# Kernel tuning notes

Measured on AMD Instinct MI355X. Metric: run time of the kernel, lower is better.

## Reference

```python
import jax, jax.numpy as jnp
import numpy as np

D = 2560
H = 64
HD = D // H  # 40
TE = 512
FF = 4 * D  # 10240
EPS = 1e-5


def _ln(x, eps=EPS):
    # fp32 layernorm, no affine
    x32 = x.astype(jnp.float32)
    mu = jnp.mean(x32, axis=-1, keepdims=True)
    var = jnp.var(x32, axis=-1, keepdims=True)
    return ((x32 - mu) * jax.lax.rsqrt(var + eps)).astype(x.dtype)


def _rope(x, cos, sin):
    # x: [B, H, S_img, HD]; cos/sin: [S_img, HD]
    half = x.shape[-1] // 2
    xr, xi = x[..., :half], x[..., half:]
    x_rot = jnp.concatenate([-xi, xr], axis=-1)
    c = cos[None, None]
    s = sin[None, None]
    return (x.astype(jnp.float32) * c + x_rot.astype(jnp.float32) * s).astype(x.dtype)


def setup_inputs() -> dict:
    key = jax.random.key(0)
    ks = jax.random.split(key, 20)
    f = jnp.float32
    inp = {
        "hidden_states": jax.random.normal(ks[0], (1, 1024, D), f),
        "encoder_hidden_states": jax.random.normal(ks[1], (1, 128, D), f),
        "time_embed": jax.random.normal(ks[2], (1, TE), f),
        "rope_cos": jax.random.uniform(ks[3], (1024, HD), f),
        "rope_sin": jax.random.uniform(ks[4], (1024, HD), f),
        # AdaLayerNormZero linear: time_embed_dim -> 12*D
        "ada_w": jax.random.normal(ks[5], (TE, 12 * D), f) * 0.02,
        "ada_b": jnp.zeros((12 * D,), f),
        # attention projections (stored [in, out])
        "wq": jax.random.normal(ks[6], (D, D), f) * 0.02,
        "bq": jnp.zeros((D,), f),
        "wk": jax.random.normal(ks[7], (D, D), f) * 0.02,
        "bk": jnp.zeros((D,), f),
        "wv": jax.random.normal(ks[8], (D, D), f) * 0.02,
        "bv": jnp.zeros((D,), f),
        "wo": jax.random.normal(ks[9], (D, D), f) * 0.02,
        "bo": jnp.zeros((D,), f),
        # feedforward (shared for img and context streams)
        "w1": jax.random.normal(ks[10], (D, FF), f) * 0.02,
        "b1": jnp.zeros((FF,), f),
        "w2": jax.random.normal(ks[11], (FF, D), f) * 0.02,
        "b2": jnp.zeros((D,), f),
    }
    return inp


def _block(hidden_states, encoder_hidden_states, time_embed, rope_cos, rope_sin,
           ada_w, ada_b, wq, bq, wk, bk, wv, bv, wo, bo, w1, b1, w2, b2):
    B, T, _ = encoder_hidden_states.shape

    # --- AdaLayerNormZero ---
    emb = time_embed @ ada_w + ada_b  # [B, 12*D]
    (shift_msa, c_shift_msa, scale_msa, c_scale_msa, gate_msa, c_gate_msa,
     shift_mlp, c_shift_mlp, scale_mlp, c_scale_mlp, gate_mlp, c_gate_mlp) = jnp.split(emb, 12, axis=1)
    u = lambda v: v[:, None, :]  # [B,1,D]

    norm_h = _ln(hidden_states) * (1 + u(scale_msa)) + u(shift_msa)
    norm_e = _ln(encoder_hidden_states) * (1 + u(c_scale_msa)) + u(c_shift_msa)

    # --- SelfAttention on concatenated [text, image] sequence ---
    x = jnp.concatenate([norm_e, norm_h], axis=1)  # [B,S,D]
    S = x.shape[1]
    def heads(y):
        return y.reshape(B, S, H, HD).transpose(0, 2, 1, 3)  # [B,H,S,HD]
    q = heads(x @ wq + bq)
    k = heads(x @ wk + bk)
    v = heads(x @ wv + bv)
    q = _ln(q)  # fp32 QK-norm over head_dim
    k = _ln(k)
    # partial RoPE on image tokens only
    q = q.at[:, :, T:, :].set(_rope(q[:, :, T:, :], rope_cos, rope_sin))
    k = k.at[:, :, T:, :].set(_rope(k[:, :, T:, :], rope_cos, rope_sin))

    scores = jnp.einsum('bhqd,bhkd->bhqk', q, k) / np.sqrt(HD).astype(np.float32)
    attn = jax.nn.softmax(scores, axis=-1)
    o = jnp.einsum('bhqk,bhkd->bhqd', attn, v)  # [B,H,S,HD]
    o = o.transpose(0, 2, 1, 3).reshape(B, S, D)
    o = o @ wo + bo
    attn_e, attn_h = o[:, :T], o[:, T:]

    # --- residual with attn gates ---
    hidden_states = hidden_states + attn_h * u(gate_msa)
    encoder_hidden_states = encoder_hidden_states + attn_e * u(c_gate_msa)

    # --- MLP with AdaLN modulation + gates ---
    nh = _ln(hidden_states) * (1 + u(scale_mlp)) + u(shift_mlp)
    ne = _ln(encoder_hidden_states) * (1 + u(c_scale_mlp)) + u(c_shift_mlp)
    ff = lambda y: jax.nn.gelu(y @ w1 + b1, approximate=True) @ w2 + b2
    hidden_states = hidden_states + ff(nh) * u(gate_mlp)
    encoder_hidden_states = encoder_hidden_states + ff(ne) * u(c_gate_mlp)
    return hidden_states, encoder_hidden_states


def reference(hidden_states, encoder_hidden_states, time_embed, rope_cos, rope_sin,
              ada_w, ada_b, wq, bq, wk, bk, wv, bv, wo, bo, w1, b1, w2, b2):
    return _block(hidden_states, encoder_hidden_states, time_embed, rope_cos, rope_sin,
                  ada_w, ada_b, wq, bq, wk, bk, wv, bv, wo, bo, w1, b1, w2, b2)
```

## Files before the change

kernel.cpp:

```cpp
#include <hip/hip_runtime.h>
#include <stdint.h>

#define D 2560
#define NH 64
#define HD 40
#define TE_ 512
#define FFD 10240
#define TENC 128
#define THID 1024
#define SEQ 1152

typedef __bf16 bf16_t;
typedef __bf16 bf16x8 __attribute__((ext_vector_type(8)));
typedef float  f32x4  __attribute__((ext_vector_type(4)));

__device__ __forceinline__ void gld_lds16(const void* g, void* l) {
  __builtin_amdgcn_global_load_lds((__attribute__((address_space(1))) void*)(g),
                                   (__attribute__((address_space(3))) void*)(l), 16, 0, 0);
}

__device__ __forceinline__ void wtrans_tile(const float* __restrict__ W, bf16_t* __restrict__ Wt,
                                            int K, int N, int bk, int bn, int tid,
                                            float* tile ) {
  #pragma unroll
  for (int i = 0; i < 4; ++i) {
    int c = i * 256 + tid;
    int r = c >> 4, q = c & 15;
    f32x4 v = *(const f32x4*)(W + (size_t)(bk * 64 + r) * N + bn * 64 + q * 4);
    tile[r * 65 + q * 4 + 0] = v[0]; tile[r * 65 + q * 4 + 1] = v[1];
    tile[r * 65 + q * 4 + 2] = v[2]; tile[r * 65 + q * 4 + 3] = v[3];
  }
  __syncthreads();
  #pragma unroll
  for (int i = 0; i < 2; ++i) {
    int c = i * 256 + tid;
    int n = c >> 3, kc = c & 7;
    bf16x8 o;
    #pragma unroll
    for (int j = 0; j < 8; ++j) o[j] = (bf16_t)tile[(kc * 8 + j) * 65 + n];
    *(bf16x8*)(Wt + (size_t)(bn * 64 + n) * K + bk * 64 + kc * 8) = o;
  }
}

__global__ __launch_bounds__(256) void prep1(
    const float* __restrict__ te, const float* __restrict__ aw, const float* __restrict__ ab,
    float* __restrict__ emb,
    const float* __restrict__ wq, const float* __restrict__ wk,
    const float* __restrict__ wv, const float* __restrict__ wo,
    bf16_t* __restrict__ wqkvT, bf16_t* __restrict__ woT,
    const float* __restrict__ bq, const float* __restrict__ bk, const float* __restrict__ bv,
    float* __restrict__ bqkv, bf16_t* __restrict__ vt) {
  __shared__ float tile[64 * 65];
  const int b = blockIdx.x, t = threadIdx.x;
  if (b < 120) {
    int j = b * 256 + t;
    float acc = ab[j];
    #pragma unroll 8
    for (int k = 0; k < TE_; ++k) acc = fmaf(te[k], aw[(size_t)k * (12 * D) + j], acc);
    emb[j] = acc;
  } else if (b < 1720) {
    int l = b - 120;  wtrans_tile(wq, wqkvT,                     D, D, l % 40, l / 40, t, tile);
  } else if (b < 3320) {
    int l = b - 1720; wtrans_tile(wk, wqkvT + (size_t)D * D,     D, D, l % 40, l / 40, t, tile);
  } else if (b < 4920) {
    int l = b - 3320; wtrans_tile(wv, wqkvT + (size_t)2 * D * D, D, D, l % 40, l / 40, t, tile);
  } else if (b < 6520) {
    int l = b - 4920; wtrans_tile(wo, woT,                       D, D, l % 40, l / 40, t, tile);
  } else if (b < 6550) {
    int i = (b - 6520) * 256 + t;
    bqkv[i] = i < D ? bq[i] : (i < 2 * D ? bk[i - D] : bv[i - 2 * D]);
  } else {
    int i = (b - 6550) * 256 + t;
    bf16x8 z = {};
    *(bf16x8*)(vt + (size_t)i * 8) = z;
  }
}

__global__ void ln_mod(const float* __restrict__ hid, const float* __restrict__ enc,
                       const float* __restrict__ emb, bf16_t* __restrict__ out,
                       int shift_h, int scale_h, int shift_e, int scale_e) {
  int row = blockIdx.x, tid = threadIdx.x;
  const float *src, *sc, *sh;
  if (row < TENC) { src = enc + (size_t)row * D;          sc = emb + scale_e * D; sh = emb + shift_e * D; }
  else            { src = hid + (size_t)(row - TENC) * D; sc = emb + scale_h * D; sh = emb + shift_h * D; }
  float v[10], s = 0.f, s2 = 0.f;
  #pragma unroll
  for (int i = 0; i < 10; ++i) { v[i] = src[tid + i * 256]; s += v[i]; s2 += v[i] * v[i]; }
  #pragma unroll
  for (int o = 32; o > 0; o >>= 1) { s += __shfl_down(s, o); s2 += __shfl_down(s2, o); }
  __shared__ float red[8];
  int wv = tid >> 6, ln = tid & 63;
  if (ln == 0) { red[wv] = s; red[4 + wv] = s2; }
  __syncthreads();
  s  = red[0] + red[1] + red[2] + red[3];
  s2 = red[4] + red[5] + red[6] + red[7];
  float mean = s * (1.f / D);
  float rstd = rsqrtf(s2 * (1.f / D) - mean * mean + 1e-5f);
  #pragma unroll
  for (int i = 0; i < 10; ++i) {
    int c = tid + i * 256;
    out[(size_t)row * D + c] = (bf16_t)((v[i] - mean) * rstd * (1.f + sc[c]) + sh[c]);
  }
}

template<int EPI>
__device__ __forceinline__ void gemm_body(
    bf16_t* As, bf16_t* Bs,
    const bf16_t* __restrict__ A, const bf16_t* __restrict__ Bt,
    const float* __restrict__ bias, int Kld, int ksteps, int N, int nM, int nMN,
    int nwg, int orig,
    float* __restrict__ outq, float* __restrict__ outk, bf16_t* __restrict__ outv,
    bf16_t* __restrict__ outb, float* __restrict__ outp) {
  const int q8 = nwg >> 3, r8 = nwg & 7;
  const int xcd = orig & 7, pos = orig >> 3;
  const int wg = (xcd < r8 ? xcd * (q8 + 1) : r8 * (q8 + 1) + (xcd - r8) * q8) + pos;
  const int part = wg / nMN, rest = wg - part * nMN;
  const int bm = rest % nM, bn = rest / nM;
  const int m0 = bm * 128, n0 = bn * 128;
  const int kbase = part * ksteps;
  const int tid = threadIdx.x, wv = tid >> 6, ln = tid & 63;
  const int wr = wv >> 1, wc = wv & 1, lr = ln & 15, lg = ln >> 4;

  f32x4 acc[4][4];
  const f32x4 zero = {0.f, 0.f, 0.f, 0.f};
  #pragma unroll
  for (int m = 0; m < 4; ++m)
    #pragma unroll
    for (int n = 0; n < 4; ++n) acc[m][n] = zero;

  for (int t = 0; t < ksteps; ++t) {
    const int k0 = (kbase + t) << 6;
    __syncthreads();
    #pragma unroll
    for (int i = 0; i < 4; ++i) {
      int g = wv * 4 + i;
      int s = g * 64 + ln;
      int r = s >> 3, ks = s & 7;
      gld_lds16(A + (size_t)(m0 + r) * Kld + k0 + ((ks ^ (r & 7)) << 3), &As[g * 512]);
    }
    #pragma unroll
    for (int i = 0; i < 4; ++i) {
      int g = wv * 4 + i;
      int s = g * 64 + ln;
      int r = s >> 3, ks = s & 7;
      gld_lds16(Bt + (size_t)(n0 + r) * Kld + k0 + ((ks ^ (r & 7)) << 3), &Bs[g * 512]);
    }
    __syncthreads();
    #pragma unroll
    for (int ks2 = 0; ks2 < 2; ++ks2) {
      int ko = ks2 * 4 + lg;
      bf16x8 af[4], bfr[4];
      #pragma unroll
      for (int m = 0; m < 4; ++m) {
        int r = wr * 64 + m * 16 + lr;
        af[m] = *(const bf16x8*)&As[r * 64 + ((ko ^ (r & 7)) << 3)];
      }
      #pragma unroll
      for (int n = 0; n < 4; ++n) {
        int c = wc * 64 + n * 16 + lr;
        bfr[n] = *(const bf16x8*)&Bs[c * 64 + ((ko ^ (c & 7)) << 3)];
      }
      #pragma unroll
      for (int m = 0; m < 4; ++m)
        #pragma unroll
        for (int n = 0; n < 4; ++n)
          acc[m][n] = __builtin_amdgcn_mfma_f32_16x16x32_bf16(af[m], bfr[n], acc[m][n], 0, 0, 0);
    }
  }

  #pragma unroll
  for (int m = 0; m < 4; ++m) {
    int row = m0 + wr * 64 + m * 16 + (lg << 2);
    #pragma unroll
    for (int n = 0; n < 4; ++n) {
      int col = n0 + wc * 64 + n * 16 + lr;
      float bv = (EPI == 4) ? 0.f : bias[col];
      #pragma unroll
      for (int r = 0; r < 4; ++r) {
        float val = acc[m][n][r] + bv;
        int rr = row + r;
        if (EPI == 0) {
          int which = col / D, cc = col - which * D;
          int h = cc / HD, dd = cc - h * HD;
          if (which == 0)      outq[(size_t)h * SEQ * HD + (size_t)rr * HD + dd] = val;
          else if (which == 1) outk[(size_t)h * SEQ * HD + (size_t)rr * HD + dd] = val;
          else                 outv[((size_t)h * 48 + dd) * SEQ + rr] = (bf16_t)val;
        } else if (EPI == 1) {
          float z = 0.7978845608028654f * (val + 0.044715f * val * val * val);
          float t2 = 1.f - 2.f / (__expf(2.f * z) + 1.f);
          outb[(size_t)rr * N + col] = (bf16_t)(0.5f * val * (1.f + t2));
        } else {
          outp[(size_t)part * SEQ * N + (size_t)rr * N + col] = val;
        }
      }
    }
  }
}

template<int EPI>
__global__ __launch_bounds__(256, 4) void gemm4(
    const bf16_t* __restrict__ A, const bf16_t* __restrict__ Bt,
    const float* __restrict__ bias, int Kld, int ksteps, int N, int nM, int nMN,
    float* __restrict__ outq, float* __restrict__ outk, bf16_t* __restrict__ outv,
    bf16_t* __restrict__ outb, float* __restrict__ outp) {
  __shared__ bf16_t As[128 * 64];
  __shared__ bf16_t Bs[128 * 64];
  gemm_body<EPI>(As, Bs, A, Bt, bias, Kld, ksteps, N, nM, nMN, gridDim.x, blockIdx.x,
                 outq, outk, outv, outb, outp);
}

__global__ __launch_bounds__(256, 4) void qkv_plus(
    const bf16_t* __restrict__ A, const bf16_t* __restrict__ wqkvT,
    const float* __restrict__ bqkv,
    float* __restrict__ outq, float* __restrict__ outk, bf16_t* __restrict__ outv,
    const float* __restrict__ w1, bf16_t* __restrict__ w1T,
    const float* __restrict__ w2, bf16_t* __restrict__ w2T) {
  __shared__ char smem[32768] __attribute__((aligned(16)));
  const int b = blockIdx.x;
  if (b < 540) {
    gemm_body<0>((bf16_t*)smem, (bf16_t*)(smem + 16384), A, wqkvT, bqkv,
                 D, 40, 3 * D, 9, 540, 540, b, outq, outk, outv, nullptr, nullptr);
  } else if (b < 6940) {
    int l = b - 540;
    wtrans_tile(w1, w1T, D, FFD, l % 40, l / 40, threadIdx.x, (float*)smem);
  } else {
    int l = b - 6940;
    wtrans_tile(w2, w2T, FFD, D, l % 160, l / 160, threadIdx.x, (float*)smem);
  }
}

template<int P>
__global__ void redk(const float* __restrict__ parts, const float* __restrict__ bias,
                     const float* __restrict__ emb, int gate_h, int gate_e,
                     const float* __restrict__ res_h, const float* __restrict__ res_e,
                     float* __restrict__ out_h, float* __restrict__ out_e) {
  int idx = blockIdx.x * 256 + threadIdx.x;
  int row = idx / (D / 4), col = (idx - row * (D / 4)) * 4;
  f32x4 s = *(const f32x4*)(bias + col);
  #pragma unroll
  for (int p = 0; p < P; ++p)
    s += *(const f32x4*)(parts + (size_t)p * SEQ * D + (size_t)row * D + col);
  const float* res; float* out; int g;
  int r2;
  if (row < TENC) { res = res_e; out = out_e; g = gate_e; r2 = row; }
  else            { res = res_h; out = out_h; g = gate_h; r2 = row - TENC; }
  f32x4 g4 = *(const f32x4*)(emb + (size_t)g * D + col);
  f32x4 rr4 = *(const f32x4*)(res + (size_t)r2 * D + col);
  f32x4 o;
  #pragma unroll
  for (int j = 0; j < 4; ++j) o[j] = rr4[j] + s[j] * g4[j];
  *(f32x4*)(out + (size_t)r2 * D + col) = o;
}

template<int P>
__global__ __launch_bounds__(256) void redk_ln(
    const float* __restrict__ parts, const float* __restrict__ bias,
    const float* __restrict__ emb, int gate_h, int gate_e,
    int shift_h, int scale_h, int shift_e, int scale_e,
    const float* __restrict__ res_h, const float* __restrict__ res_e,
    float* __restrict__ out_h, float* __restrict__ out_e, bf16_t* __restrict__ xout) {
  int row = blockIdx.x, tid = threadIdx.x;
  const float* res; float* out; int g, sh, sc; int r2;
  if (row < TENC) { res = res_e; out = out_e; g = gate_e; sh = shift_e; sc = scale_e; r2 = row; }
  else            { res = res_h; out = out_h; g = gate_h; sh = shift_h; sc = scale_h; r2 = row - TENC; }
  float v[10], s = 0.f, s2 = 0.f;
  #pragma unroll
  for (int i = 0; i < 10; ++i) {
    int c = tid + i * 256;
    float val = bias[c];
    #pragma unroll
    for (int p = 0; p < P; ++p) val += parts[(size_t)p * SEQ * D + (size_t)row * D + c];
    val = res[(size_t)r2 * D + c] + val * emb[(size_t)g * D + c];
    out[(size_t)r2 * D + c] = val;
    v[i] = val; s += val; s2 += val * val;
  }
  #pragma unroll
  for (int o = 32; o > 0; o >>= 1) { s += __shfl_down(s, o); s2 += __shfl_down(s2, o); }
  __shared__ float red[8];
  int wvv = tid >> 6, lnn = tid & 63;
  if (lnn == 0) { red[wvv] = s; red[4 + wvv] = s2; }
  __syncthreads();
  s  = red[0] + red[1] + red[2] + red[3];
  s2 = red[4] + red[5] + red[6] + red[7];
  float mean = s * (1.f / D);
  float rstd = rsqrtf(s2 * (1.f / D) - mean * mean + 1e-5f);
  #pragma unroll
  for (int i = 0; i < 10; ++i) {
    int c = tid + i * 256;
    xout[(size_t)row * D + c] =
        (bf16_t)((v[i] - mean) * rstd * (1.f + emb[(size_t)sc * D + c]) + emb[(size_t)sh * D + c]);
  }
}

__global__ void qk_post(const float* __restrict__ qh, const float* __restrict__ kh,
                        const float* __restrict__ rc, const float* __restrict__ rs,
                        bf16_t* __restrict__ qb, bf16_t* __restrict__ kb) {
  int r = blockIdx.x * 128 + threadIdx.x;
  int h = blockIdx.y;
  float cs[HD], sn[HD];
  bool rope = (r >= TENC);
  if (rope) {
    const float* cp = rc + (size_t)(r - TENC) * HD;
    const float* sp = rs + (size_t)(r - TENC) * HD;
    #pragma unroll
    for (int d = 0; d < HD; ++d) { cs[d] = cp[d]; sn[d] = sp[d]; }
  }
  #pragma unroll
  for (int which = 0; which < 2; ++which) {
    const float* base = (which == 0 ? qh : kh) + (size_t)h * SEQ * HD + (size_t)r * HD;
    bf16_t* dst = (which == 0 ? qb : kb) + ((size_t)h * SEQ + r) * 64;
    float v[HD], s = 0.f, s2 = 0.f;
    #pragma unroll
    for (int d = 0; d < HD; ++d) { v[d] = base[d]; s += v[d]; }
    float mean = s * (1.f / HD);
    #pragma unroll
    for (int d = 0; d < HD; ++d) { float x = v[d] - mean; v[d] = x; s2 += x * x; }
    float rstd = rsqrtf(s2 * (1.f / HD) + 1e-5f);
    #pragma unroll
    for (int d = 0; d < HD; ++d) v[d] *= rstd;
    if (rope) {
      #pragma unroll
      for (int d = 0; d < HD / 2; ++d) {
        float lo = v[d], hi = v[d + 20];
        v[d]      = lo * cs[d]      - hi * sn[d];
        v[d + 20] = hi * cs[d + 20] + lo * sn[d + 20];
      }
    }
    float qs = (which == 0) ? 0.15811388300841897f : 1.f;
    #pragma unroll
    for (int d = 0; d < HD; ++d) dst[d] = (bf16_t)(v[d] * qs);
    #pragma unroll
    for (int d = HD; d < 64; ++d) dst[d] = (bf16_t)0.f;
  }
}

__global__ __launch_bounds__(256) void attn_mfma(
    const bf16_t* __restrict__ qb, const bf16_t* __restrict__ kb,
    const bf16_t* __restrict__ vt, bf16_t* __restrict__ obf) {
  __shared__ bf16_t Ks[64 * 64];
  __shared__ bf16_t Vs[48 * 64];
  __shared__ bf16_t Ps[4][16 * 64];
  const int h = blockIdx.y;
  const int tid = threadIdx.x, wv = tid >> 6, ln = tid & 63;
  const int qbase = blockIdx.x * 64 + wv * 16;
  const int lr = ln & 15, lg = ln >> 4;

  bf16x8 af[2];
  {
    const bf16_t* qp = qb + ((size_t)h * SEQ + qbase + lr) * 64 + lg * 8;
    af[0] = *(const bf16x8*)(qp);
    af[1] = *(const bf16x8*)(qp + 32);
  }
  const f32x4 zero = {0.f, 0.f, 0.f, 0.f};
  f32x4 acc[3];
  acc[0] = zero; acc[1] = zero; acc[2] = zero;
  float mrow[4], lrow[4];
  #pragma unroll
  for (int r = 0; r < 4; ++r) { mrow[r] = -1e30f; lrow[r] = 0.f; }

  const bf16_t* kbh = kb + (size_t)h * SEQ * 64;
  const bf16_t* vth = vt + (size_t)h * 48 * SEQ;

  for (int kv0 = 0; kv0 < SEQ; kv0 += 64) {
    __syncthreads();
    #pragma unroll
    for (int i = 0; i < 2; ++i) {
      int g = wv * 2 + i;
      int slot = g * 64 + ln;
      int kr = slot >> 3, so = slot & 7;
      gld_lds16(kbh + (size_t)(kv0 + kr) * 64 + ((so ^ (kr & 7)) << 3), &Ks[g * 512]);
    }
    #pragma unroll
    for (int i = 0; i < 2; ++i) {
      int g = wv + 4 * i;
      if (g < 6) {
        int slot = g * 64 + ln;
        int dr = slot >> 3, so = slot & 7;
        gld_lds16(vth + (size_t)dr * SEQ + kv0 + ((so ^ (dr & 7)) << 3), &Vs[g * 512]);
      }
    }
    __syncthreads();
    f32x4 s[4];
    #pragma unroll
    for (int nt = 0; nt < 4; ++nt) {
      s[nt] = zero;
      int kvr = nt * 16 + lr;
      #pragma unroll
      for (int kk = 0; kk < 2; ++kk) {
        bf16x8 bk = *(const bf16x8*)&Ks[kvr * 64 + (((kk * 4 + lg) ^ (kvr & 7)) << 3)];
        s[nt] = __builtin_amdgcn_mfma_f32_16x16x32_bf16(af[kk], bk, s[nt], 0, 0, 0);
      }
    }
    float pn[4][4];
    #pragma unroll
    for (int r = 0; r < 4; ++r) {
      float tm = fmaxf(fmaxf(s[0][r], s[1][r]), fmaxf(s[2][r], s[3][r]));
      #pragma unroll
      for (int o = 8; o > 0; o >>= 1) tm = fmaxf(tm, __shfl_xor(tm, o));
      float mn = fmaxf(mrow[r], tm);
      float scl = __expf(mrow[r] - mn);
      mrow[r] = mn;
      float ts = 0.f;
      #pragma unroll
      for (int nt = 0; nt < 4; ++nt) { pn[nt][r] = __expf(s[nt][r] - mn); ts += pn[nt][r]; }
      #pragma unroll
      for (int o = 8; o > 0; o >>= 1) ts += __shfl_xor(ts, o);
      lrow[r] = lrow[r] * scl + ts;
      acc[0][r] *= scl; acc[1][r] *= scl; acc[2][r] *= scl;
    }
    #pragma unroll
    for (int nt = 0; nt < 4; ++nt)
      #pragma unroll
      for (int r = 0; r < 4; ++r) {
        int q = lg * 4 + r;
        int kv = nt * 16 + lr;
        Ps[wv][q * 64 + ((((kv >> 3) ^ (q & 7)) << 3) | (kv & 7))] = (bf16_t)pn[nt][r];
      }
    bf16x8 pa[2];
    #pragma unroll
    for (int kk = 0; kk < 2; ++kk)
      pa[kk] = *(const bf16x8*)&Ps[wv][lr * 64 + (((kk * 4 + lg) ^ (lr & 7)) << 3)];
    #pragma unroll
    for (int dt = 0; dt < 3; ++dt) {
      #pragma unroll
      for (int kk = 0; kk < 2; ++kk) {
        int dr = dt * 16 + lr;
        bf16x8 bv = *(const bf16x8*)&Vs[dr * 64 + (((kk * 4 + lg) ^ (dr & 7)) << 3)];
        acc[dt] = __builtin_amdgcn_mfma_f32_16x16x32_bf16(pa[kk], bv, acc[dt], 0, 0, 0);
      }
    }
  }
  #pragma unroll
  for (int dt = 0; dt < 3; ++dt) {
    int d = dt * 16 + lr;
    if (d < HD) {
      #pragma unroll
      for (int r = 0; r < 4; ++r) {
        int q = qbase + lg * 4 + r;
        obf[(size_t)q * D + h * HD + d] = (bf16_t)(acc[dt][r] / lrow[r]);
      }
    }
  }
}

extern "C" void kernel_launch(void* const* d_in, const int* in_sizes, int n_in,
                              void* d_out, int out_size, void* d_ws, size_t ws_size,
                              hipStream_t stream) {
  const float* hid = (const float*)d_in[0];
  const float* enc = (const float*)d_in[1];
  const float* tem = (const float*)d_in[2];
  const float* rc  = (const float*)d_in[3];
  const float* rs  = (const float*)d_in[4];
  const float* aw  = (const float*)d_in[5];
  const float* ab  = (const float*)d_in[6];
  const float* wq  = (const float*)d_in[7];
  const float* bq  = (const float*)d_in[8];
  const float* wk  = (const float*)d_in[9];
  const float* bk  = (const float*)d_in[10];
  const float* wvv = (const float*)d_in[11];
  const float* bv  = (const float*)d_in[12];
  const float* wo  = (const float*)d_in[13];
  const float* bo  = (const float*)d_in[14];
  const float* w1  = (const float*)d_in[15];
  const float* b1  = (const float*)d_in[16];
  const float* w2  = (const float*)d_in[17];
  const float* b2  = (const float*)d_in[18];
  float* out_hid = (float*)d_out;
  float* out_enc = out_hid + (size_t)THID * D;

  char* ws = (char*)d_ws;
  size_t off = 0;
  auto alloc = [&](size_t b) { char* p = ws + off; off += (b + 255) & ~(size_t)255; return p; };
  float*  emb  = (float*) alloc((size_t)12 * D * 4);
  bf16_t* xln  = (bf16_t*)alloc((size_t)SEQ * D * 2);
  float*  qh   = (float*) alloc((size_t)NH * SEQ * HD * 4);
  float*  kh   = (float*) alloc((size_t)NH * SEQ * HD * 4);
  bf16_t* vt   = (bf16_t*)alloc((size_t)NH * 48 * SEQ * 2);
  bf16_t* qbb  = (bf16_t*)alloc((size_t)NH * SEQ * 64 * 2);
  bf16_t* kbb  = (bf16_t*)alloc((size_t)NH * SEQ * 64 * 2);
  bf16_t* wqkvT= (bf16_t*)alloc((size_t)3 * D * D * 2);
  bf16_t* woT  = (bf16_t*)alloc((size_t)D * D * 2);
  bf16_t* w1T  = (bf16_t*)alloc((size_t)FFD * D * 2);
  bf16_t* w2T  = (bf16_t*)alloc((size_t)D * FFD * 2);
  float*  bqkv = (float*) alloc((size_t)3 * D * 4);
  bf16_t* obf = xln;
  bf16_t* aff = (bf16_t*)qh;
  float*  h1  = (float*)qbb;
  float*  e1  = h1 + (size_t)THID * D;
  float*  oparts = (float*)wqkvT;
  float*  fparts = (float*)wqkvT;

  prep1<<<dim3(8278), dim3(256), 0, stream>>>(tem, aw, ab, emb, wq, wk, wvv, wo,
      wqkvT, woT, bq, bk, bv, bqkv, vt);
  ln_mod<<<dim3(SEQ), dim3(256), 0, stream>>>(hid, enc, emb, xln, 0, 2, 1, 3);
  qkv_plus<<<dim3(13340), dim3(256), 0, stream>>>(xln, wqkvT, bqkv, qh, kh, vt,
      w1, w1T, w2, w2T);
  qk_post<<<dim3(9, 64), dim3(128), 0, stream>>>(qh, kh, rc, rs, qbb, kbb);
  attn_mfma<<<dim3(18, 64), dim3(256), 0, stream>>>(qbb, kbb, vt, obf);
  gemm4<4><<<dim3(360), dim3(256), 0, stream>>>(obf, woT, nullptr, D, 20, D, 9, 180,
      nullptr, nullptr, nullptr, nullptr, oparts);
  redk_ln<2><<<dim3(SEQ), dim3(256), 0, stream>>>(oparts, bo, emb, 4, 5, 6, 8, 7, 9,
      hid, enc, h1, e1, xln);
  gemm4<1><<<dim3(720), dim3(256), 0, stream>>>(xln, w1T, b1, D, 40, FFD, 9, 720,
      nullptr, nullptr, nullptr, aff, nullptr);
  gemm4<4><<<dim3(720), dim3(256), 0, stream>>>(aff, w2T, nullptr, FFD, 40, D, 9, 180,
      nullptr, nullptr, nullptr, nullptr, fparts);
  redk<4><<<dim3(2880), dim3(256), 0, stream>>>(fparts, b2, emb, 10, 11, h1, e1, out_hid, out_enc);
}
```

Baseline: 475.1 us.

## Split-K QKV GEMM, fuse QK-norm/RoPE reduction, and rebalance weight transposes across kernels

The QKV GEMM now uses a two-way split-K, which doubles its workgroup count, and writes fp32 partial sums. A new row-wise kernel sums the partials, adds the bias, and applies per-head layernorm, RoPE, Q scaling and bf16 packing, replacing the old scattered epilogue and the separate qk_post kernel. The Wo transpose moves into the QKV launch, and the W1/W2 transposes are folded into the attention launch so they overlap with attention work. The split-K adds extra fp32 partial traffic, and qparts reuses the w1T buffer, so correctness depends on w1T being written only after qkv_red has consumed it.

```diff
diff --git a/kernel.cpp b/kernel.cpp
--- a/kernel.cpp
+++ b/kernel.cpp
@@ -45,9 +45,8 @@
 __global__ __launch_bounds__(256) void prep1(
     const float* __restrict__ te, const float* __restrict__ aw, const float* __restrict__ ab,
     float* __restrict__ emb,
-    const float* __restrict__ wq, const float* __restrict__ wk,
-    const float* __restrict__ wv, const float* __restrict__ wo,
-    bf16_t* __restrict__ wqkvT, bf16_t* __restrict__ woT,
+    const float* __restrict__ wq, const float* __restrict__ wk, const float* __restrict__ wv,
+    bf16_t* __restrict__ wqkvT,
     const float* __restrict__ bq, const float* __restrict__ bk, const float* __restrict__ bv,
     float* __restrict__ bqkv, bf16_t* __restrict__ vt) {
   __shared__ float tile[64 * 65];
@@ -64,15 +63,14 @@
     int l = b - 1720; wtrans_tile(wk, wqkvT + (size_t)D * D,     D, D, l % 40, l / 40, t, tile);
   } else if (b < 4920) {
     int l = b - 3320; wtrans_tile(wv, wqkvT + (size_t)2 * D * D, D, D, l % 40, l / 40, t, tile);
-  } else if (b < 6520) {
-    int l = b - 4920; wtrans_tile(wo, woT,                       D, D, l % 40, l / 40, t, tile);
-  } else if (b < 6550) {
-    int i = (b - 6520) * 256 + t;
+  } else if (b < 4950) {
+    int i = (b - 4920) * 256 + t;
     bqkv[i] = i < D ? bq[i] : (i < 2 * D ? bk[i - D] : bv[i - 2 * D]);
   } else {
-    int i = (b - 6550) * 256 + t;
+    int i = (b - 4950) * 256 + t;
+    int h = i / 1152, g = i - h * 1152;
     bf16x8 z = {};
-    *(bf16x8*)(vt + (size_t)i * 8) = z;
+    *(bf16x8*)(vt + ((size_t)h * 48 + 40) * SEQ + g * 8) = z;
   }
 }
 
@@ -109,7 +107,6 @@
     const bf16_t* __restrict__ A, const bf16_t* __restrict__ Bt,
     const float* __restrict__ bias, int Kld, int ksteps, int N, int nM, int nMN,
     int nwg, int orig,
-    float* __restrict__ outq, float* __restrict__ outk, bf16_t* __restrict__ outv,
     bf16_t* __restrict__ outb, float* __restrict__ outp) {
   const int q8 = nwg >> 3, r8 = nwg & 7;
   const int xcd = orig & 7, pos = orig >> 3;
@@ -179,13 +176,7 @@
       for (int r = 0; r < 4; ++r) {
         float val = acc[m][n][r] + bv;
         int rr = row + r;
-        if (EPI == 0) {
-          int which = col / D, cc = col - which * D;
-          int h = cc / HD, dd = cc - h * HD;
-          if (which == 0)      outq[(size_t)h * SEQ * HD + (size_t)rr * HD + dd] = val;
-          else if (which == 1) outk[(size_t)h * SEQ * HD + (size_t)rr * HD + dd] = val;
-          else                 outv[((size_t)h * 48 + dd) * SEQ + rr] = (bf16_t)val;
-        } else if (EPI == 1) {
+        if (EPI == 1) {
           float z = 0.7978845608028654f * (val + 0.044715f * val * val * val);
           float t2 = 1.f - 2.f / (__expf(2.f * z) + 1.f);
           outb[(size_t)rr * N + col] = (bf16_t)(0.5f * val * (1.f + t2));
@@ -201,31 +192,93 @@
 __global__ __launch_bounds__(256, 4) void gemm4(
     const bf16_t* __restrict__ A, const bf16_t* __restrict__ Bt,
     const float* __restrict__ bias, int Kld, int ksteps, int N, int nM, int nMN,
-    float* __restrict__ outq, float* __restrict__ outk, bf16_t* __restrict__ outv,
     bf16_t* __restrict__ outb, float* __restrict__ outp) {
   __shared__ bf16_t As[128 * 64];
   __shared__ bf16_t Bs[128 * 64];
   gemm_body<EPI>(As, Bs, A, Bt, bias, Kld, ksteps, N, nM, nMN, gridDim.x, blockIdx.x,
-                 outq, outk, outv, outb, outp);
-}
-
-__global__ __launch_bounds__(256, 4) void qkv_plus(
+                 outb, outp);
+}
+
+__global__ __launch_bounds__(256, 4) void qkv_g(
     const bf16_t* __restrict__ A, const bf16_t* __restrict__ wqkvT,
-    const float* __restrict__ bqkv,
-    float* __restrict__ outq, float* __restrict__ outk, bf16_t* __restrict__ outv,
-    const float* __restrict__ w1, bf16_t* __restrict__ w1T,
-    const float* __restrict__ w2, bf16_t* __restrict__ w2T) {
+    float* __restrict__ qparts,
+    const float* __restrict__ wo, bf16_t* __restrict__ woT) {
   __shared__ char smem[32768] __attribute__((aligned(16)));
   const int b = blockIdx.x;
-  if (b < 540) {
-    gemm_body<0>((bf16_t*)smem, (bf16_t*)(smem + 16384), A, wqkvT, bqkv,
-                 D, 40, 3 * D, 9, 540, 540, b, outq, outk, outv, nullptr, nullptr);
-  } else if (b < 6940) {
-    int l = b - 540;
-    wtrans_tile(w1, w1T, D, FFD, l % 40, l / 40, threadIdx.x, (float*)smem);
+  if (b < 1080) {
+    gemm_body<4>((bf16_t*)smem, (bf16_t*)(smem + 16384), A, wqkvT, nullptr,
+                 D, 20, 3 * D, 9, 540, 1080, b, nullptr, qparts);
   } else {
-    int l = b - 6940;
-    wtrans_tile(w2, w2T, FFD, D, l % 160, l / 160, threadIdx.x, (float*)smem);
+    int l = b - 1080;
+    wtrans_tile(wo, woT, D, D, l % 40, l / 40, threadIdx.x, (float*)smem);
+  }
+}
+
+__global__ __launch_bounds__(256) void qkv_red(
+    const float* __restrict__ parts, const float* __restrict__ bqkv,
+    const float* __restrict__ rc, const float* __restrict__ rs,
+    bf16_t* __restrict__ qb, bf16_t* __restrict__ kb, bf16_t* __restrict__ vt) {
+  const int r = blockIdx.x, t = threadIdx.x;
+  const int h = t >> 2, sub = t & 3;
+  __shared__ float cs_s[HD], sn_s[HD];
+  const bool rope = (r >= TENC);
+  if (rope && t < 2 * HD) {
+    if (t < HD) cs_s[t] = rc[(size_t)(r - TENC) * HD + t];
+    else        sn_s[t - HD] = rs[(size_t)(r - TENC) * HD + (t - HD)];
+  }
+  const float* p0 = parts + (size_t)r * (3 * D);
+  const float* p1 = p0 + (size_t)SEQ * (3 * D);
+  const int cq = h * HD + sub * 10;
+  float q[10], k[10], v[10];
+  #pragma unroll
+  for (int j = 0; j < 10; ++j) {
+    q[j] = p0[cq + j] + p1[cq + j] + bqkv[cq + j];
+    k[j] = p0[D + cq + j] + p1[D + cq + j] + bqkv[D + cq + j];
+    v[j] = p0[2 * D + cq + j] + p1[2 * D + cq + j] + bqkv[2 * D + cq + j];
+  }
+  __syncthreads();
+  float qs = 0.f, qs2 = 0.f, ks = 0.f, ks2 = 0.f;
+  #pragma unroll
+  for (int j = 0; j < 10; ++j) { qs += q[j]; qs2 += q[j] * q[j]; ks += k[j]; ks2 += k[j] * k[j]; }
+  qs += __shfl_xor(qs, 1); qs += __shfl_xor(qs, 2);
+  qs2 += __shfl_xor(qs2, 1); qs2 += __shfl_xor(qs2, 2);
+  ks += __shfl_xor(ks, 1); ks += __shfl_xor(ks, 2);
+  ks2 += __shfl_xor(ks2, 1); ks2 += __shfl_xor(ks2, 2);
+  float qm = qs * (1.f / HD), km = ks * (1.f / HD);
+  float qr = rsqrtf(qs2 * (1.f / HD) - qm * qm + 1e-5f);
+  float kr = rsqrtf(ks2 * (1.f / HD) - km * km + 1e-5f);
+  #pragma unroll
+  for (int j = 0; j < 10; ++j) { q[j] = (q[j] - qm) * qr; k[j] = (k[j] - km) * kr; }
+  if (rope) {
+    float pq[10], pk[10];
+    #pragma unroll
+    for (int j = 0; j < 10; ++j) { pq[j] = __shfl_xor(q[j], 2); pk[j] = __shfl_xor(k[j], 2); }
+    #pragma unroll
+    for (int j = 0; j < 10; ++j) {
+      int d = sub * 10 + j;
+      float c = cs_s[d], s = sn_s[d];
+      if (d < 20) { q[j] = q[j] * c - pq[j] * s; k[j] = k[j] * c - pk[j] * s; }
+      else        { q[j] = q[j] * c + pq[j] * s; k[j] = k[j] * c + pk[j] * s; }
+    }
+  }
+  bf16_t* qd = qb + ((size_t)h * SEQ + r) * 64;
+  bf16_t* kd = kb + ((size_t)h * SEQ + r) * 64;
+  const float qscale = 0.15811388300841897f;
+  #pragma unroll
+  for (int j = 0; j < 10; ++j) {
+    int d = sub * 10 + j;
+    qd[d] = (bf16_t)(q[j] * qscale);
+    kd[d] = (bf16_t)k[j];
+  }
+  #pragma unroll
+  for (int j = 0; j < 6; ++j) {
+    int d = 40 + sub * 6 + j;
+    qd[d] = (bf16_t)0.f; kd[d] = (bf16_t)0.f;
+  }
+  #pragma unroll
+  for (int j = 0; j < 10; ++j) {
+    int d = sub * 10 + j;
+    vt[((size_t)h * 48 + d) * SEQ + r] = (bf16_t)v[j];
   }
 }
 
@@ -292,57 +345,25 @@
   }
 }
 
-__global__ void qk_post(const float* __restrict__ qh, const float* __restrict__ kh,
-                        const float* __restrict__ rc, const float* __restrict__ rs,
-                        bf16_t* __restrict__ qb, bf16_t* __restrict__ kb) {
-  int r = blockIdx.x * 128 + threadIdx.x;
-  int h = blockIdx.y;
-  float cs[HD], sn[HD];
-  bool rope = (r >= TENC);
-  if (rope) {
-    const float* cp = rc + (size_t)(r - TENC) * HD;
-    const float* sp = rs + (size_t)(r - TENC) * HD;
-    #pragma unroll
-    for (int d = 0; d < HD; ++d) { cs[d] = cp[d]; sn[d] = sp[d]; }
-  }
-  #pragma unroll
-  for (int which = 0; which < 2; ++which) {
-    const float* base = (which == 0 ? qh : kh) + (size_t)h * SEQ * HD + (size_t)r * HD;
-    bf16_t* dst = (which == 0 ? qb : kb) + ((size_t)h * SEQ + r) * 64;
-    float v[HD], s = 0.f, s2 = 0.f;
-    #pragma unroll
-    for (int d = 0; d < HD; ++d) { v[d] = base[d]; s += v[d]; }
-    float mean = s * (1.f / HD);
-    #pragma unroll
-    for (int d = 0; d < HD; ++d) { float x = v[d] - mean; v[d] = x; s2 += x * x; }
-    float rstd = rsqrtf(s2 * (1.f / HD) + 1e-5f);
-    #pragma unroll
-    for (int d = 0; d < HD; ++d) v[d] *= rstd;
-    if (rope) {
-      #pragma unroll
-      for (int d = 0; d < HD / 2; ++d) {
-        float lo = v[d], hi = v[d + 20];
-        v[d]      = lo * cs[d]      - hi * sn[d];
-        v[d + 20] = hi * cs[d + 20] + lo * sn[d + 20];
-      }
-    }
-    float qs = (which == 0) ? 0.15811388300841897f : 1.f;
-    #pragma unroll
-    for (int d = 0; d < HD; ++d) dst[d] = (bf16_t)(v[d] * qs);
-    #pragma unroll
-    for (int d = HD; d < 64; ++d) dst[d] = (bf16_t)0.f;
-  }
-}
-
-__global__ __launch_bounds__(256) void attn_mfma(
+__global__ __launch_bounds__(256) void attn_plus(
     const bf16_t* __restrict__ qb, const bf16_t* __restrict__ kb,
-    const bf16_t* __restrict__ vt, bf16_t* __restrict__ obf) {
-  __shared__ bf16_t Ks[64 * 64];
-  __shared__ bf16_t Vs[48 * 64];
-  __shared__ bf16_t Ps[4][16 * 64];
-  const int h = blockIdx.y;
+    const bf16_t* __restrict__ vt, bf16_t* __restrict__ obf,
+    const float* __restrict__ w1, bf16_t* __restrict__ w1T,
+    const float* __restrict__ w2, bf16_t* __restrict__ w2T) {
+  __shared__ char smem[22528] __attribute__((aligned(16)));
+  const int b = blockIdx.x;
+  if (b >= 1152) {
+    if (b < 7552) { int l = b - 1152; wtrans_tile(w1, w1T, D, FFD, l % 40, l / 40, threadIdx.x, (float*)smem); }
+    else          { int l = b - 7552; wtrans_tile(w2, w2T, FFD, D, l % 160, l / 160, threadIdx.x, (float*)smem); }
+    return;
+  }
+  bf16_t* Ks = (bf16_t*)smem;
+  bf16_t* Vs = (bf16_t*)(smem + 8192);
+  bf16_t* Ps = (bf16_t*)(smem + 14336);
+  const int h = b & 63;
+  const int qblk = b >> 6;
   const int tid = threadIdx.x, wv = tid >> 6, ln = tid & 63;
-  const int qbase = blockIdx.x * 64 + wv * 16;
+  const int qbase = qblk * 64 + wv * 16;
   const int lr = ln & 15, lg = ln >> 4;
 
   bf16x8 af[2];
@@ -414,12 +435,12 @@
       for (int r = 0; r < 4; ++r) {
         int q = lg * 4 + r;
         int kv = nt * 16 + lr;
-        Ps[wv][q * 64 + ((((kv >> 3) ^ (q & 7)) << 3) | (kv & 7))] = (bf16_t)pn[nt][r];
+        Ps[wv * 1024 + q * 64 + ((((kv >> 3) ^ (q & 7)) << 3) | (kv & 7))] = (bf16_t)pn[nt][r];
       }
     bf16x8 pa[2];
     #pragma unroll
     for (int kk = 0; kk < 2; ++kk)
-      pa[kk] = *(const bf16x8*)&Ps[wv][lr * 64 + (((kk * 4 + lg) ^ (lr & 7)) << 3)];
+      pa[kk] = *(const bf16x8*)&Ps[wv * 1024 + lr * 64 + (((kk * 4 + lg) ^ (lr & 7)) << 3)];
     #pragma unroll
     for (int dt = 0; dt < 3; ++dt) {
       #pragma unroll
@@ -473,8 +494,7 @@
   auto alloc = [&](size_t b) { char* p = ws + off; off += (b + 255) & ~(size_t)255; return p; };
   float*  emb  = (float*) alloc((size_t)12 * D * 4);
   bf16_t* xln  = (bf16_t*)alloc((size_t)SEQ * D * 2);
-  float*  qh   = (float*) alloc((size_t)NH * SEQ * HD * 4);
-  float*  kh   = (float*) alloc((size_t)NH * SEQ * HD * 4);
+  bf16_t* aff  = (bf16_t*)alloc((size_t)SEQ * FFD * 2);
   bf16_t* vt   = (bf16_t*)alloc((size_t)NH * 48 * SEQ * 2);
   bf16_t* qbb  = (bf16_t*)alloc((size_t)NH * SEQ * 64 * 2);
   bf16_t* kbb  = (bf16_t*)alloc((size_t)NH * SEQ * 64 * 2);
@@ -484,26 +504,25 @@
   bf16_t* w2T  = (bf16_t*)alloc((size_t)D * FFD * 2);
   float*  bqkv = (float*) alloc((size_t)3 * D * 4);
   bf16_t* obf = xln;
-  bf16_t* aff = (bf16_t*)qh;
   float*  h1  = (float*)qbb;
   float*  e1  = h1 + (size_t)THID * D;
+  float*  qparts = (float*)w1T;
   float*  oparts = (float*)wqkvT;
   float*  fparts = (float*)wqkvT;
 
-  prep1<<<dim3(8278), dim3(256), 0, stream>>>(tem, aw, ab, emb, wq, wk, wvv, wo,
-      wqkvT, woT, bq, bk, bv, bqkv, vt);
+  prep1<<<dim3(5238), dim3(256), 0, stream>>>(tem, aw, ab, emb, wq, wk, wvv,
+      wqkvT, bq, bk, bv, bqkv, vt);
   ln_mod<<<dim3(SEQ), dim3(256), 0, stream>>>(hid, enc, emb, xln, 0, 2, 1, 3);
-  qkv_plus<<<dim3(13340), dim3(256), 0, stream>>>(xln, wqkvT, bqkv, qh, kh, vt,
-      w1, w1T, w2, w2T);
-  qk_post<<<dim3(9, 64), dim3(128), 0, stream>>>(qh, kh, rc, rs, qbb, kbb);
-  attn_mfma<<<dim3(18, 64), dim3(256), 0, stream>>>(qbb, kbb, vt, obf);
+  qkv_g<<<dim3(2680), dim3(256), 0, stream>>>(xln, wqkvT, qparts, wo, woT);
+  qkv_red<<<dim3(SEQ), dim3(256), 0, stream>>>(qparts, bqkv, rc, rs, qbb, kbb, vt);
+  attn_plus<<<dim3(13952), dim3(256), 0, stream>>>(qbb, kbb, vt, obf, w1, w1T, w2, w2T);
   gemm4<4><<<dim3(360), dim3(256), 0, stream>>>(obf, woT, nullptr, D, 20, D, 9, 180,
-      nullptr, nullptr, nullptr, nullptr, oparts);
+      nullptr, oparts);
   redk_ln<2><<<dim3(SEQ), dim3(256), 0, stream>>>(oparts, bo, emb, 4, 5, 6, 8, 7, 9,
       hid, enc, h1, e1, xln);
   gemm4<1><<<dim3(720), dim3(256), 0, stream>>>(xln, w1T, b1, D, 40, FFD, 9, 720,
-      nullptr, nullptr, nullptr, aff, nullptr);
+      aff, nullptr);
   gemm4<4><<<dim3(720), dim3(256), 0, stream>>>(aff, w2T, nullptr, FFD, 40, D, 9, 180,
-      nullptr, nullptr, nullptr, nullptr, fparts);
+      nullptr, fparts);
   redk<4><<<dim3(2880), dim3(256), 0, stream>>>(fparts, b2, emb, 10, 11, h1, e1, out_hid, out_enc);
 }
```

Result: no change. 480.6 us (+1.2%).
